# Kernel tuning notes

Measured on AMD Instinct MI355X. Metric: run time of the kernel, lower is better.

Reference implementation:

```python
import jax, jax.numpy as jnp
import numpy as np

N = 10000
E = 320000
D = 256
EPS = 1e-5

def layer_norm(x, g, b):
    mu = jnp.mean(x, axis=-1, keepdims=True)
    var = jnp.mean(jnp.square(x - mu), axis=-1, keepdims=True)
    return (x - mu) * jax.lax.rsqrt(var + EPS) * g + b

def linear(x, w, b):
    # w: [in, out]
    return x @ w + b

def setup_inputs() -> dict:
    key = jax.random.key(0)
    ks = jax.random.split(key, 20)
    s = 1.0 / np.sqrt(D)
    inp = {
        'x': jax.random.normal(ks[0], (N, D), jnp.float32),
        'edge_index': jax.random.randint(ks[1], (2, E), 0, N, jnp.int64),
        'edge_weight': jax.random.normal(ks[2], (E,), jnp.float32),
        'wq': jax.random.normal(ks[3], (D, D), jnp.float32) * s,
        'bq': jnp.zeros((D,), jnp.float32),
        'wk': jax.random.normal(ks[4], (D, D), jnp.float32) * s,
        'bk': jnp.zeros((D,), jnp.float32),
        'wv': jax.random.normal(ks[5], (D, D), jnp.float32) * s,
        'bv': jnp.zeros((D,), jnp.float32),
        'ws': jax.random.normal(ks[6], (D, D), jnp.float32) * s,
        'bs': jnp.zeros((D,), jnp.float32),
        'we': jax.random.normal(ks[7], (1, 1), jnp.float32),
        'be': jnp.zeros((1,), jnp.float32),
        'g1': jnp.ones((D,), jnp.float32),
        'b1': jnp.zeros((D,), jnp.float32),
        'g2': jnp.ones((D,), jnp.float32),
        'b2': jnp.zeros((D,), jnp.float32),
        'w_ff1': jax.random.normal(ks[8], (D, 2 * D), jnp.float32) * s,
        'b_ff1': jnp.zeros((2 * D,), jnp.float32),
        'w_ff2': jax.random.normal(ks[9], (2 * D, D), jnp.float32) * (1.0 / np.sqrt(2 * D)),
        'b_ff2': jnp.zeros((D,), jnp.float32),
    }
    return inp

def reference(x, edge_index, edge_weight, wq, bq, wk, bk, wv, bv, ws, bs, we, be,
              g1, b1, g2, b2, w_ff1, b_ff1, w_ff2, b_ff2):
    n = x.shape[0]
    scale = x.shape[-1] ** (-0.5)
    q = linear(x, wq, bq)
    k = linear(x, wk, bk)
    v = linear(x, wv, bv)
    src, dst = edge_index[0], edge_index[1]
    # per-edge attention scores: dot(q[dst], k[src]) * scale
    scores = jnp.sum(q[dst] * k[src], axis=-1) * scale
    scores = scores + (edge_weight[:, None] @ we + be)[:, 0]
    # two-pass segment softmax over dst
    seg_max = jax.ops.segment_max(scores, dst, num_segments=n)
    exp_s = jnp.exp(scores - seg_max[dst])
    denom = jax.ops.segment_sum(exp_s, dst, num_segments=n)
    attn = exp_s / jnp.maximum(denom[dst], 1e-12)
    # scatter-add weighted messages
    message = v[src] * attn[:, None]  # [E, D]
    out = jax.ops.segment_sum(message, dst, num_segments=n)
    x = layer_norm(x + out + linear(x, ws, bs), g1, b1)
    ffn = linear(jax.nn.gelu(linear(x, w_ff1, b_ff1)), w_ff2, b_ff2)
    x = layer_norm(x + ffn, g2, b2)
    return x
```

## Files before the change

kernel.cpp:

```cpp
#include <hip/hip_runtime.h>
#include <math.h>

#define N_NODES 10000
#define N_EDGES 320000
#define DIM 256
#define BCAP 128

#define P_PARTS 250
#define NPP 40
#define PCAP 2048
#define EPT 16

typedef __attribute__((ext_vector_type(8))) short bf16x8;
typedef __attribute__((ext_vector_type(4))) float fx4;

typedef __attribute__((address_space(3))) unsigned lds_u32;
typedef __attribute__((address_space(1))) const unsigned gbl_u32;


__device__ __forceinline__ float gelu_tanh(float x) {
  const float k0 = 0.7978845608028654f;
  float x3 = x * x * x;
  return 0.5f * x * (1.0f + tanhf(k0 * (x + 0.044715f * x3)));
}

__device__ __forceinline__ unsigned short f2bf(float f) {
  unsigned u = __float_as_uint(f);
  unsigned r = 0x7FFFu + ((u >> 16) & 1u);
  return (unsigned short)((u + r) >> 16);
}

__device__ __forceinline__ float bf_lo(unsigned u) { return __uint_as_float(u << 16); }
__device__ __forceinline__ float bf_hi(unsigned u) { return __uint_as_float(u & 0xFFFF0000u); }


#define SEG_QKVS 262144
#define SEG_FF1 131072
#define SEG_FF2 131072
#define SEG_BIAS 1024
#define SEG_CONV 320000
#define SEG_ZCNT 256
#define PREP_TOTAL (SEG_QKVS + SEG_FF1 + SEG_FF2 + SEG_BIAS + SEG_CONV + SEG_ZCNT)

__global__ __launch_bounds__(256) void prep_all_kernel(
    const float* __restrict__ wq, const float* __restrict__ wk,
    const float* __restrict__ wv, const float* __restrict__ ws,
    const float* __restrict__ bq, const float* __restrict__ bk,
    const float* __restrict__ bv, const float* __restrict__ bs,
    const float* __restrict__ wff1, const float* __restrict__ wff2,
    const float* __restrict__ x,
    unsigned short* __restrict__ wt_qkvs, float* __restrict__ bias_qkvs,
    unsigned short* __restrict__ wt_ff1, unsigned short* __restrict__ wt_ff2,
    unsigned short* __restrict__ xb, unsigned* __restrict__ pcnt) {
  int id = blockIdx.x * 256 + threadIdx.x;
  if (id < SEG_QKVS) {
    const int n = id >> 8, k = id & 255;
    const float* w = (n < 256) ? wq : (n < 512) ? wk : (n < 768) ? wv : ws;
    wt_qkvs[id] = f2bf(w[k * 256 + (n & 255)]);
    return;
  }
  id -= SEG_QKVS;
  if (id < SEG_FF1) {
    const int n = id >> 8, k = id & 255;
    wt_ff1[id] = f2bf(wff1[k * 512 + n]);
    return;
  }
  id -= SEG_FF1;
  if (id < SEG_FF2) {
    const int n = id >> 9, k = id & 511;
    wt_ff2[id] = f2bf(wff2[k * 256 + n]);
    return;
  }
  id -= SEG_FF2;
  if (id < SEG_BIAS) {
    bias_qkvs[id] = (id < 256) ? bq[id] : (id < 512) ? bk[id & 255]
                    : (id < 768) ? bv[id & 255] : bs[id & 255];
    return;
  }
  id -= SEG_BIAS;
  if (id < SEG_CONV) {
    const int base = id * 8;
    float4 a = *(const float4*)(x + base);
    float4 b = *(const float4*)(x + base + 4);
    unsigned short h[8] = {f2bf(a.x), f2bf(a.y), f2bf(a.z), f2bf(a.w),
                           f2bf(b.x), f2bf(b.y), f2bf(b.z), f2bf(b.w)};
    *(uint4*)(xb + base) = *(const uint4*)h;
    return;
  }
  id -= SEG_CONV;
  if (id < SEG_ZCNT) pcnt[id] = 0u;
}

__global__ __launch_bounds__(512) void scatter_p1(
    const int* __restrict__ ei, const float* __restrict__ ew,
    const float* __restrict__ we, const float* __restrict__ be,
    unsigned* __restrict__ pcnt, uint2* __restrict__ pbuf) {
  __shared__ unsigned lcnt[P_PARTS];
  __shared__ unsigned lbase[P_PARTS];
  const int tid = threadIdx.x;
  for (int i = tid; i < P_PARTS; i += 512) lcnt[i] = 0;
  __syncthreads();
  const float wes = we[0], bes = be[0];
  const int e0 = blockIdx.x * (512 * EPT);

  unsigned pp[EPT];
  unsigned rr[EPT];
  unsigned sv[EPT];
  float ebv[EPT];
#pragma unroll
  for (int j = 0; j < EPT; j++) {
    const int e = e0 + j * 512 + tid;
    pp[j] = 0;
    rr[j] = 0xFFFFFFFFu;
    if (e < N_EDGES) {
      const int dst = ei[N_EDGES + e];
      const int src = ei[e];
      const int p = dst / NPP;
      sv[j] = (unsigned)dst | ((unsigned)src << 16);
      ebv[j] = fmaf(ew[e], wes, bes);
      pp[j] = (unsigned)p;
      rr[j] = atomicAdd(&lcnt[p], 1u);
    }
  }
  __syncthreads();
  for (int i = tid; i < P_PARTS; i += 512) {
    const unsigned c = lcnt[i];
    lbase[i] = c ? atomicAdd(&pcnt[i], c) : 0u;
  }
  __syncthreads();
#pragma unroll
  for (int j = 0; j < EPT; j++) {
    if (rr[j] != 0xFFFFFFFFu) {
      const unsigned pos = lbase[pp[j]] + rr[j];
      if (pos < PCAP) {
        uint2 rec;
        rec.x = sv[j];
        rec.y = __float_as_uint(ebv[j]);
        pbuf[(size_t)pp[j] * PCAP + pos] = rec;
      }
    }
  }
}

__global__ __launch_bounds__(256) void scatter_p2(
    const unsigned* __restrict__ pcnt, const uint2* __restrict__ pbuf,
    unsigned* __restrict__ cnt, uint2* __restrict__ es_csr) {
  __shared__ unsigned lcnt[NPP];
  const int p = blockIdx.x;
  const int tid = threadIdx.x;
  if (tid < NPP) lcnt[tid] = 0;
  __syncthreads();
  const int n0 = p * NPP;
  const int tot = min((int)pcnt[p], PCAP);
  for (int i = tid; i < tot; i += 256) {
    const uint2 rec = pbuf[(size_t)p * PCAP + i];
    const int dst = (int)(rec.x & 0xFFFFu);
    const int src = (int)(rec.x >> 16);
    const unsigned r = atomicAdd(&lcnt[dst - n0], 1u);
    if (r < BCAP) {
      uint2 o;
      o.x = (unsigned)src;
      o.y = rec.y;
      es_csr[(size_t)dst * BCAP + r] = o;
    }
  }
  __syncthreads();
  if (tid < NPP) cnt[n0 + tid] = lcnt[tid];
}

template <int GELU, int WF32, int WB16, int SPLIT>
__global__ __launch_bounds__(256) void mfma_gemm(
    const unsigned short* __restrict__ A, int lda,
    const unsigned short* __restrict__ Bt,
    const float* __restrict__ bias,
    const float* __restrict__ xres,
    float* __restrict__ C, int ldc,
    unsigned short* __restrict__ Cb, int ldcb,
    int M, int K) {
  __shared__ char lds[65536];
  const int tid = threadIdx.x;

  const int l = tid & 63;
  const int wid = tid >> 6;
  const int wrow = (wid & 1) * 64;
  const int wcol = (wid >> 1) * 64;
  const int bm = blockIdx.y * 128;
  const int bn = blockIdx.x * 128;

  fx4 acc[4][4];
#pragma unroll
  for (int i = 0; i < 4; i++)
#pragma unroll
    for (int j = 0; j < 4; j++) acc[i][j] = (fx4)(0.0f);

#define STAGE(BUFOFF, KB)                                                      \
  {                                                                            \
    _Pragma("unroll") for (int i = 0; i < 4; i++) {                            \
      const int id = i * 256 + tid;                                            \
      const int row = id >> 3;                                                 \
      const int ccs = (id & 7) ^ (row & 7);                                    \
      __builtin_amdgcn_global_load_lds(                                        \
          (gbl_u32*)(A + (size_t)(bm + row) * lda + (KB) + ccs * 8),           \
          (lds_u32*)(lds + (BUFOFF) + id * 16), 16, 0, 0);                     \
    }                                                                          \
    _Pragma("unroll") for (int i = 0; i < 4; i++) {                            \
      const int id = i * 256 + tid;                                            \
      const int row = id >> 3;                                                 \
      const int ccs = (id & 7) ^ (row & 7);                                    \
      __builtin_amdgcn_global_load_lds(                                        \
          (gbl_u32*)(Bt + (size_t)(bn + row) * K + (KB) + ccs * 8),            \
          (lds_u32*)(lds + (BUFOFF) + 16384 + id * 16), 16, 0, 0);             \
    }                                                                          \
  }

  STAGE(0, 0);

  unsigned cur = 0;
  for (int kb = 0; kb < K; kb += 64) {
    if (kb + 64 < K) {
      STAGE((cur ^ 1) * 32768, kb + 64);
      asm volatile("s_waitcnt vmcnt(8)" ::: "memory");
    } else {
      asm volatile("s_waitcnt vmcnt(0)" ::: "memory");
    }
    __builtin_amdgcn_s_barrier();
    __builtin_amdgcn_sched_barrier(0);

    const char* As = lds + cur * 32768;
    const char* Bs = As + 16384;
#pragma unroll
    for (int kk = 0; kk < 2; kk++) {
      const int kbyte = (kk * 64 + ((l >> 4) << 4)) ^ ((l & 7) << 4);
      bf16x8 af[4], bg[4];
#pragma unroll
      for (int f = 0; f < 4; f++) {
        const int ar = wrow + f * 16 + (l & 15);
        af[f] = *(const bf16x8*)(As + ar * 128 + kbyte);
        const int br = wcol + f * 16 + (l & 15);
        bg[f] = *(const bf16x8*)(Bs + br * 128 + kbyte);
      }
#pragma unroll
      for (int fr = 0; fr < 4; fr++)
#pragma unroll
        for (int fc = 0; fc < 4; fc++)
          acc[fr][fc] = __builtin_amdgcn_mfma_f32_16x16x32_bf16(
              bg[fc], af[fr], acc[fr][fc], 0, 0, 0);
    }
    __builtin_amdgcn_s_barrier();
    cur ^= 1;
  }
#undef STAGE

  const int seg = bn >> 8;
#pragma unroll
  for (int fr = 0; fr < 4; fr++) {
    const int m = bm + wrow + fr * 16 + (l & 15);
    if (m < M) {
#pragma unroll
      for (int fc = 0; fc < 4; fc++) {
        const int n0 = bn + wcol + fc * 16 + ((l >> 4) << 2);
        const float4 b4 = *(const float4*)(bias + n0);
        fx4 v = acc[fr][fc];
        float o0 = v[0] + b4.x;
        float o1 = v[1] + b4.y;
        float o2 = v[2] + b4.z;
        float o3 = v[3] + b4.w;
        if (GELU) {
          o0 = gelu_tanh(o0); o1 = gelu_tanh(o1);
          o2 = gelu_tanh(o2); o3 = gelu_tanh(o3);
        }
        if (SPLIT) {
          const int nn = n0 & 255;
          if (seg == 3) {
            const float4 xr = *(const float4*)(xres + (size_t)m * 256 + nn);
            float4 w;
            w.x = o0 + xr.x; w.y = o1 + xr.y; w.z = o2 + xr.z; w.w = o3 + xr.w;
            *(float4*)(C + (size_t)m * 256 + nn) = w;
          } else {
            uint2 pk;
            pk.x = (unsigned)f2bf(o0) | ((unsigned)f2bf(o1) << 16);
            pk.y = (unsigned)f2bf(o2) | ((unsigned)f2bf(o3) << 16);
            *(uint2*)(Cb + (size_t)seg * (N_NODES * DIM) + (size_t)m * 256 + nn) = pk;
          }
        } else {
          if (WF32) {
            float4 w; w.x = o0; w.y = o1; w.z = o2; w.w = o3;
            *(float4*)(C + (size_t)m * ldc + n0) = w;
          }
          if (WB16) {
            uint2 pk;
            pk.x = (unsigned)f2bf(o0) | ((unsigned)f2bf(o1) << 16);
            pk.y = (unsigned)f2bf(o2) | ((unsigned)f2bf(o3) << 16);
            *(uint2*)(Cb + (size_t)m * ldcb + n0) = pk;
          }
        }
      }
    }
  }
}

__global__ __launch_bounds__(64) void agg_fused_kernel(
    const unsigned* __restrict__ cnt, const uint2* __restrict__ es_csr,
    const unsigned short* __restrict__ qb,
    const unsigned short* __restrict__ kb, const unsigned short* __restrict__ vb,
    const float* __restrict__ sbuf,
    const float* __restrict__ g, const float* __restrict__ b,
    float* __restrict__ out, unsigned short* __restrict__ outb) {
  const int node = blockIdx.x;
  const int lane = threadIdx.x;
  const int grp = lane >> 4;
  const int t = lane & 15;
  const int start = node * BCAP;
  const int deg = min((int)cnt[node], BCAP);
  const int end = start + deg;

  const uint4 qA = *(const uint4*)(qb + (size_t)node * 256 + t * 16);
  const uint4 qB = *(const uint4*)(qb + (size_t)node * 256 + t * 16 + 8);
  float qf[16];
  qf[0] = bf_lo(qA.x);  qf[1] = bf_hi(qA.x);
  qf[2] = bf_lo(qA.y);  qf[3] = bf_hi(qA.y);
  qf[4] = bf_lo(qA.z);  qf[5] = bf_hi(qA.z);
  qf[6] = bf_lo(qA.w);  qf[7] = bf_hi(qA.w);
  qf[8] = bf_lo(qB.x);  qf[9] = bf_hi(qB.x);
  qf[10] = bf_lo(qB.y); qf[11] = bf_hi(qB.y);
  qf[12] = bf_lo(qB.z); qf[13] = bf_hi(qB.z);
  qf[14] = bf_lo(qB.w); qf[15] = bf_hi(qB.w);

  float m = -3.4e38f, dsum = 0.f;
  float a0 = 0.f, a1 = 0.f, a2 = 0.f, a3 = 0.f;

  int ea = start + grp * 2;
  int eb_ = ea + 1;
  bool va = ea < end, vbd = eb_ < end;
  int sa = 0, sb = 0;
  float ba = 0.f, bb = 0.f;
  if (va) { const uint2 es = es_csr[ea]; sa = (int)es.x; ba = __uint_as_float(es.y); }
  if (vbd) { const uint2 es = es_csr[eb_]; sb = (int)es.x; bb = __uint_as_float(es.y); }
  uint4 kAa = *(const uint4*)(kb + (size_t)sa * 256 + t * 16);
  uint4 kBa = *(const uint4*)(kb + (size_t)sa * 256 + t * 16 + 8);
  uint4 kAb = *(const uint4*)(kb + (size_t)sb * 256 + t * 16);
  uint4 kBb = *(const uint4*)(kb + (size_t)sb * 256 + t * 16 + 8);

  for (int base = start; base < end; base += 8) {
    const int s0 = __shfl(sa, 0), s1 = __shfl(sa, 16);
    const int s2 = __shfl(sa, 32), s3 = __shfl(sa, 48);
    const int s4 = __shfl(sb, 0), s5 = __shfl(sb, 16);
    const int s6 = __shfl(sb, 32), s7 = __shfl(sb, 48);
    const uint2 v0 = *(const uint2*)(vb + (size_t)s0 * 256 + lane * 4);
    const uint2 v1 = *(const uint2*)(vb + (size_t)s1 * 256 + lane * 4);
    const uint2 v2 = *(const uint2*)(vb + (size_t)s2 * 256 + lane * 4);
    const uint2 v3 = *(const uint2*)(vb + (size_t)s3 * 256 + lane * 4);
    const uint2 v4 = *(const uint2*)(vb + (size_t)s4 * 256 + lane * 4);
    const uint2 v5 = *(const uint2*)(vb + (size_t)s5 * 256 + lane * 4);
    const uint2 v6 = *(const uint2*)(vb + (size_t)s6 * 256 + lane * 4);
    const uint2 v7 = *(const uint2*)(vb + (size_t)s7 * 256 + lane * 4);

    const int na = base + 8 + grp * 2;
    const int nb = na + 1;
    const bool va_n = na < end, vb_n = nb < end;
    int sa_n = 0, sb_n = 0;
    float ba_n = 0.f, bb_n = 0.f;
    if (va_n) { const uint2 es = es_csr[na]; sa_n = (int)es.x; ba_n = __uint_as_float(es.y); }
    if (vb_n) { const uint2 es = es_csr[nb]; sb_n = (int)es.x; bb_n = __uint_as_float(es.y); }

    float da = qf[0] * bf_lo(kAa.x);
    float db = qf[0] * bf_lo(kAb.x);
    da = fmaf(qf[1], bf_hi(kAa.x), da);  db = fmaf(qf[1], bf_hi(kAb.x), db);
    da = fmaf(qf[2], bf_lo(kAa.y), da);  db = fmaf(qf[2], bf_lo(kAb.y), db);
    da = fmaf(qf[3], bf_hi(kAa.y), da);  db = fmaf(qf[3], bf_hi(kAb.y), db);
    da = fmaf(qf[4], bf_lo(kAa.z), da);  db = fmaf(qf[4], bf_lo(kAb.z), db);
    da = fmaf(qf[5], bf_hi(kAa.z), da);  db = fmaf(qf[5], bf_hi(kAb.z), db);
    da = fmaf(qf[6], bf_lo(kAa.w), da);  db = fmaf(qf[6], bf_lo(kAb.w), db);
    da = fmaf(qf[7], bf_hi(kAa.w), da);  db = fmaf(qf[7], bf_hi(kAb.w), db);
    da = fmaf(qf[8], bf_lo(kBa.x), da);  db = fmaf(qf[8], bf_lo(kBb.x), db);
    da = fmaf(qf[9], bf_hi(kBa.x), da);  db = fmaf(qf[9], bf_hi(kBb.x), db);
    da = fmaf(qf[10], bf_lo(kBa.y), da); db = fmaf(qf[10], bf_lo(kBb.y), db);
    da = fmaf(qf[11], bf_hi(kBa.y), da); db = fmaf(qf[11], bf_hi(kBb.y), db);
    da = fmaf(qf[12], bf_lo(kBa.z), da); db = fmaf(qf[12], bf_lo(kBb.z), db);
    da = fmaf(qf[13], bf_hi(kBa.z), da); db = fmaf(qf[13], bf_hi(kBb.z), db);
    da = fmaf(qf[14], bf_lo(kBa.w), da); db = fmaf(qf[14], bf_lo(kBb.w), db);
    da = fmaf(qf[15], bf_hi(kBa.w), da); db = fmaf(qf[15], bf_hi(kBb.w), db);
    da += __shfl_xor(da, 1);  db += __shfl_xor(db, 1);
    da += __shfl_xor(da, 2);  db += __shfl_xor(db, 2);
    da += __shfl_xor(da, 4);  db += __shfl_xor(db, 4);
    da += __shfl_xor(da, 8);  db += __shfl_xor(db, 8);
    const float sca = va ? fmaf(da, 0.0625f, ba) : -3.4e38f;
    const float scb = vbd ? fmaf(db, 0.0625f, bb) : -3.4e38f;

    const uint4 kAa_n = *(const uint4*)(kb + (size_t)sa_n * 256 + t * 16);
    const uint4 kBa_n = *(const uint4*)(kb + (size_t)sa_n * 256 + t * 16 + 8);
    const uint4 kAb_n = *(const uint4*)(kb + (size_t)sb_n * 256 + t * 16);
    const uint4 kBb_n = *(const uint4*)(kb + (size_t)sb_n * 256 + t * 16 + 8);

    const float c0 = __shfl(sca, 0), c1 = __shfl(sca, 16);
    const float c2 = __shfl(sca, 32), c3 = __shfl(sca, 48);
    const float c4 = __shfl(scb, 0), c5 = __shfl(scb, 16);
    const float c6 = __shfl(scb, 32), c7 = __shfl(scb, 48);

    const float mx = fmaxf(fmaxf(fmaxf(c0, c1), fmaxf(c2, c3)),
                           fmaxf(fmaxf(c4, c5), fmaxf(c6, c7)));
    const float mn = fmaxf(m, mx);
    const float scale = __expf(m - mn);
    const float w0 = __expf(c0 - mn), w1 = __expf(c1 - mn);
    const float w2 = __expf(c2 - mn), w3 = __expf(c3 - mn);
    const float w4 = __expf(c4 - mn), w5 = __expf(c5 - mn);
    const float w6 = __expf(c6 - mn), w7 = __expf(c7 - mn);
    dsum = fmaf(dsum, scale, ((w0 + w1) + (w2 + w3)) + ((w4 + w5) + (w6 + w7)));

    float t0 = a0 * scale;
    t0 = fmaf(w0, bf_lo(v0.x), t0); t0 = fmaf(w1, bf_lo(v1.x), t0);
    t0 = fmaf(w2, bf_lo(v2.x), t0); t0 = fmaf(w3, bf_lo(v3.x), t0);
    t0 = fmaf(w4, bf_lo(v4.x), t0); t0 = fmaf(w5, bf_lo(v5.x), t0);
    t0 = fmaf(w6, bf_lo(v6.x), t0); t0 = fmaf(w7, bf_lo(v7.x), t0);
    a0 = t0;
    float t1 = a1 * scale;
    t1 = fmaf(w0, bf_hi(v0.x), t1); t1 = fmaf(w1, bf_hi(v1.x), t1);
    t1 = fmaf(w2, bf_hi(v2.x), t1); t1 = fmaf(w3, bf_hi(v3.x), t1);
    t1 = fmaf(w4, bf_hi(v4.x), t1); t1 = fmaf(w5, bf_hi(v5.x), t1);
    t1 = fmaf(w6, bf_hi(v6.x), t1); t1 = fmaf(w7, bf_hi(v7.x), t1);
    a1 = t1;
    float t2 = a2 * scale;
    t2 = fmaf(w0, bf_lo(v0.y), t2); t2 = fmaf(w1, bf_lo(v1.y), t2);
    t2 = fmaf(w2, bf_lo(v2.y), t2); t2 = fmaf(w3, bf_lo(v3.y), t2);
    t2 = fmaf(w4, bf_lo(v4.y), t2); t2 = fmaf(w5, bf_lo(v5.y), t2);
    t2 = fmaf(w6, bf_lo(v6.y), t2); t2 = fmaf(w7, bf_lo(v7.y), t2);
    a2 = t2;
    float t3 = a3 * scale;
    t3 = fmaf(w0, bf_hi(v0.y), t3); t3 = fmaf(w1, bf_hi(v1.y), t3);
    t3 = fmaf(w2, bf_hi(v2.y), t3); t3 = fmaf(w3, bf_hi(v3.y), t3);
    t3 = fmaf(w4, bf_hi(v4.y), t3); t3 = fmaf(w5, bf_hi(v5.y), t3);
    t3 = fmaf(w6, bf_hi(v6.y), t3); t3 = fmaf(w7, bf_hi(v7.y), t3);
    a3 = t3;
    m = mn;

    sa = sa_n; sb = sb_n;
    ba = ba_n; bb = bb_n;
    va = va_n; vbd = vb_n;
    kAa = kAa_n; kBa = kBa_n;
    kAb = kAb_n; kBb = kBb_n;
  }
  const float inv = 1.0f / fmaxf(dsum, 1e-12f);

  const float4 sv = *(const float4*)(sbuf + (size_t)node * 256 + lane * 4);
  float r0 = a0 * inv + sv.x;
  float r1 = a1 * inv + sv.y;
  float r2 = a2 * inv + sv.z;
  float r3 = a3 * inv + sv.w;

  float sum = r0 + r1 + r2 + r3;
#pragma unroll
  for (int off = 32; off > 0; off >>= 1) sum += __shfl_xor(sum, off);
  const float mu = sum * (1.0f / 256.0f);
  const float d0 = r0 - mu, d1 = r1 - mu, d2 = r2 - mu, d3 = r3 - mu;
  float vs = d0 * d0 + d1 * d1 + d2 * d2 + d3 * d3;
#pragma unroll
  for (int off = 32; off > 0; off >>= 1) vs += __shfl_xor(vs, off);
  const float rs = rsqrtf(vs * (1.0f / 256.0f) + 1e-5f);

  const float4 gv = *(const float4*)(g + lane * 4);
  const float4 bv = *(const float4*)(b + lane * 4);
  float4 o;
  o.x = d0 * rs * gv.x + bv.x;
  o.y = d1 * rs * gv.y + bv.y;
  o.z = d2 * rs * gv.z + bv.z;
  o.w = d3 * rs * gv.w + bv.w;
  *(float4*)(out + (size_t)node * 256 + lane * 4) = o;
  uint2 pk;
  pk.x = (unsigned)f2bf(o.x) | ((unsigned)f2bf(o.y) << 16);
  pk.y = (unsigned)f2bf(o.z) | ((unsigned)f2bf(o.w) << 16);
  *(uint2*)(outb + (size_t)node * 256 + lane * 4) = pk;
}


__global__ __launch_bounds__(256) void ln2_kernel(
    const float* __restrict__ x1, const float* __restrict__ y,
    const float* __restrict__ g, const float* __restrict__ b,
    float* __restrict__ out) {
  __shared__ float red[4];
  const int row = blockIdx.x;
  const int t = threadIdx.x;
  float v = x1[(size_t)row * 256 + t] + y[(size_t)row * 256 + t];
  float s = v;
#pragma unroll
  for (int off = 32; off > 0; off >>= 1) s += __shfl_xor(s, off);
  if ((t & 63) == 0) red[t >> 6] = s;
  __syncthreads();
  float tot = red[0] + red[1] + red[2] + red[3];
  __syncthreads();
  const float mu = tot * (1.0f / 256.0f);
  const float d = v - mu;
  float vs = d * d;
#pragma unroll
  for (int off = 32; off > 0; off >>= 1) vs += __shfl_xor(vs, off);
  if ((t & 63) == 0) red[t >> 6] = vs;
  __syncthreads();
  float vtot = red[0] + red[1] + red[2] + red[3];
  const float r = rsqrtf(vtot * (1.0f / 256.0f) + 1e-5f);
  out[(size_t)row * 256 + t] = d * r * g[t] + b[t];
}


extern "C" void kernel_launch(void* const* d_in, const int* in_sizes, int n_in,
                              void* d_out, int out_size, void* d_ws,
                              size_t ws_size, hipStream_t stream) {
  const float* x = (const float*)d_in[0];
  const int* ei = (const int*)d_in[1];
  const float* ew = (const float*)d_in[2];
  const float* wq = (const float*)d_in[3];
  const float* bq = (const float*)d_in[4];
  const float* wk = (const float*)d_in[5];
  const float* bk = (const float*)d_in[6];
  const float* wv = (const float*)d_in[7];
  const float* bv = (const float*)d_in[8];
  const float* wsm = (const float*)d_in[9];
  const float* bs = (const float*)d_in[10];
  const float* we = (const float*)d_in[11];
  const float* be = (const float*)d_in[12];
  const float* g1 = (const float*)d_in[13];
  const float* b1 = (const float*)d_in[14];
  const float* g2 = (const float*)d_in[15];
  const float* b2 = (const float*)d_in[16];
  const float* wff1 = (const float*)d_in[17];
  const float* bff1 = (const float*)d_in[18];
  const float* wff2 = (const float*)d_in[19];
  const float* bff2 = (const float*)d_in[20];
  float* out = (float*)d_out;

  unsigned short* qb = (unsigned short*)d_ws;
  unsigned short* kbp = qb + 2560000;
  unsigned short* vbp = qb + 5120000;
  float* sbuf = (float*)(qb + 7680000);
  uint2* es_csr = (uint2*)(sbuf + 2560000);
  unsigned* cnt = (unsigned*)(es_csr + (size_t)N_NODES * BCAP);
  float* x1 = (float*)(cnt + N_NODES);
  float* y = x1 + 2560000;
  unsigned short* x1b = (unsigned short*)(y + 2560000);
  unsigned short* h_b = x1b + 2560000;
  unsigned short* xb = h_b;
  unsigned short* wt_qkvs = h_b + 5120000;
  unsigned short* wt_ff1 = wt_qkvs + 262144;
  unsigned short* wt_ff2 = wt_ff1 + 131072;
  float* bias_qkvs = (float*)(wt_ff2 + 131072);
  unsigned* pcnt = (unsigned*)(bias_qkvs + 1024);
  uint2* pbuf = (uint2*)(pcnt + 256);

  dim3 blk(256);
  const int mb = (N_NODES + 127) / 128;

  prep_all_kernel<<<(PREP_TOTAL + 255) / 256, blk, 0, stream>>>(
      wq, wk, wv, wsm, bq, bk, bv, bs, wff1, wff2, x,
      wt_qkvs, bias_qkvs, wt_ff1, wt_ff2, xb, pcnt);

  scatter_p1<<<(N_EDGES + 512 * EPT - 1) / (512 * EPT), dim3(512), 0, stream>>>(
      ei, ew, we, be, pcnt, pbuf);
  scatter_p2<<<P_PARTS, blk, 0, stream>>>(pcnt, pbuf, cnt, es_csr);

  mfma_gemm<0, 0, 0, 1><<<dim3(8, mb), blk, 0, stream>>>(
      xb, 256, wt_qkvs, bias_qkvs, x, sbuf, 0, qb, 0, N_NODES, 256);

  agg_fused_kernel<<<N_NODES, dim3(64), 0, stream>>>(
      cnt, es_csr, qb, kbp, vbp, sbuf, g1, b1, x1, x1b);

  mfma_gemm<1, 0, 1, 0><<<dim3(4, mb), blk, 0, stream>>>(
      x1b, 256, wt_ff1, bff1, nullptr, (float*)nullptr, 0, h_b, 512, N_NODES, 256);

  mfma_gemm<0, 1, 0, 0><<<dim3(2, mb), blk, 0, stream>>>(
      h_b, 512, wt_ff2, bff2, nullptr, y, 256, (unsigned short*)nullptr, 0, N_NODES, 512);

  ln2_kernel<<<N_NODES, blk, 0, stream>>>(x1, y, g2, b2, out);
}
```

Measured before the change: 133.6 us.

## Use 64x64 split-K MFMA GEMM for FFN2 with reduction fused into LN2

Replaces the 128-row-tile FFN2 GEMM (only 2x79 blocks) with a 64x64-tile kernel that splits K=512 into two halves across blockIdx.z, giving 4x157x2 blocks for better CU occupancy. Each half writes a separate fp32 partial, with bias applied only in the first, and ln2 sums both partials. This adds a 10MB partial write and an extra read in LN2. The last row tile reads past N_NODES in A (10000 is not a multiple of 64), though stores are guarded.

```diff
diff --git a/kernel.cpp b/kernel.cpp
--- a/kernel.cpp
+++ b/kernel.cpp
@@ -299,6 +299,108 @@
   }
 }
 
+__global__ __launch_bounds__(256) void mfma_gemm64_splitk(
+    const unsigned short* __restrict__ A, int lda,
+    const unsigned short* __restrict__ Bt, int ldb,
+    const float* __restrict__ bias,
+    float* __restrict__ C,
+    int M, int kLen) {
+  __shared__ char lds[32768];
+  const int tid = threadIdx.x;
+  const int l = tid & 63;
+  const int wid = tid >> 6;
+  const int wrow = (wid & 1) * 32;
+  const int wcol = (wid >> 1) * 32;
+  const int bm = blockIdx.y * 64;
+  const int bn = blockIdx.x * 64;
+  const int kOff = blockIdx.z * kLen;
+  const float bmul = (blockIdx.z == 0) ? 1.0f : 0.0f;
+  float* Cz = C + (size_t)blockIdx.z * (N_NODES * DIM);
+
+  fx4 acc[2][2];
+#pragma unroll
+  for (int i = 0; i < 2; i++)
+#pragma unroll
+    for (int j = 0; j < 2; j++) acc[i][j] = (fx4)(0.0f);
+
+#define STAGE64(BUFOFF, KB)                                                    \
+  {                                                                            \
+    _Pragma("unroll") for (int i = 0; i < 2; i++) {                            \
+      const int id = i * 256 + tid;                                            \
+      const int row = id >> 3;                                                 \
+      const int ccs = (id & 7) ^ (row & 7);                                    \
+      __builtin_amdgcn_global_load_lds(                                        \
+          (gbl_u32*)(A + (size_t)(bm + row) * lda + kOff + (KB) + ccs * 8),    \
+          (lds_u32*)(lds + (BUFOFF) + id * 16), 16, 0, 0);                     \
+    }                                                                          \
+    _Pragma("unroll") for (int i = 0; i < 2; i++) {                            \
+      const int id = i * 256 + tid;                                            \
+      const int row = id >> 3;                                                 \
+      const int ccs = (id & 7) ^ (row & 7);                                    \
+      __builtin_amdgcn_global_load_lds(                                        \
+          (gbl_u32*)(Bt + (size_t)(bn + row) * ldb + kOff + (KB) + ccs * 8),   \
+          (lds_u32*)(lds + (BUFOFF) + 8192 + id * 16), 16, 0, 0);              \
+    }                                                                          \
+  }
+
+  STAGE64(0, 0);
+
+  unsigned cur = 0;
+  for (int kb = 0; kb < kLen; kb += 64) {
+    if (kb + 64 < kLen) {
+      STAGE64((cur ^ 1) * 16384, kb + 64);
+      asm volatile("s_waitcnt vmcnt(4)" ::: "memory");
+    } else {
+      asm volatile("s_waitcnt vmcnt(0)" ::: "memory");
+    }
+    __builtin_amdgcn_s_barrier();
+    __builtin_amdgcn_sched_barrier(0);
+
+    const char* As = lds + cur * 16384;
+    const char* Bs = As + 8192;
+#pragma unroll
+    for (int kk = 0; kk < 2; kk++) {
+      const int kbyte = (kk * 64 + ((l >> 4) << 4)) ^ ((l & 7) << 4);
+      bf16x8 af[2], bg[2];
+#pragma unroll
+      for (int f = 0; f < 2; f++) {
+        const int ar = wrow + f * 16 + (l & 15);
+        af[f] = *(const bf16x8*)(As + ar * 128 + kbyte);
+        const int br = wcol + f * 16 + (l & 15);
+        bg[f] = *(const bf16x8*)(Bs + br * 128 + kbyte);
+      }
+#pragma unroll
+      for (int fr = 0; fr < 2; fr++)
+#pragma unroll
+        for (int fc = 0; fc < 2; fc++)
+          acc[fr][fc] = __builtin_amdgcn_mfma_f32_16x16x32_bf16(
+              bg[fc], af[fr], acc[fr][fc], 0, 0, 0);
+    }
+    __builtin_amdgcn_s_barrier();
+    cur ^= 1;
+  }
+#undef STAGE64
+
+#pragma unroll
+  for (int fr = 0; fr < 2; fr++) {
+    const int m = bm + wrow + fr * 16 + (l & 15);
+    if (m < M) {
+#pragma unroll
+      for (int fc = 0; fc < 2; fc++) {
+        const int n0 = bn + wcol + fc * 16 + ((l >> 4) << 2);
+        const float4 b4 = *(const float4*)(bias + n0);
+        fx4 v = acc[fr][fc];
+        float4 w;
+        w.x = fmaf(b4.x, bmul, v[0]);
+        w.y = fmaf(b4.y, bmul, v[1]);
+        w.z = fmaf(b4.z, bmul, v[2]);
+        w.w = fmaf(b4.w, bmul, v[3]);
+        *(float4*)(Cz + (size_t)m * DIM + n0) = w;
+      }
+    }
+  }
+}
+
 __global__ __launch_bounds__(64) void agg_fused_kernel(
     const unsigned* __restrict__ cnt, const uint2* __restrict__ es_csr,
     const unsigned short* __restrict__ qb,
@@ -474,12 +576,14 @@
 
 __global__ __launch_bounds__(256) void ln2_kernel(
     const float* __restrict__ x1, const float* __restrict__ y,
+    const float* __restrict__ y2,
     const float* __restrict__ g, const float* __restrict__ b,
     float* __restrict__ out) {
   __shared__ float red[4];
   const int row = blockIdx.x;
   const int t = threadIdx.x;
-  float v = x1[(size_t)row * 256 + t] + y[(size_t)row * 256 + t];
+  const size_t idx = (size_t)row * 256 + t;
+  float v = x1[idx] + y[idx] + y2[idx];
   float s = v;
 #pragma unroll
   for (int off = 32; off > 0; off >>= 1) s += __shfl_xor(s, off);
@@ -496,7 +600,7 @@
   __syncthreads();
   float vtot = red[0] + red[1] + red[2] + red[3];
   const float r = rsqrtf(vtot * (1.0f / 256.0f) + 1e-5f);
-  out[(size_t)row * 256 + t] = d * r * g[t] + b[t];
+  out[idx] = d * r * g[t] + b[t];
 }
 
 
@@ -543,9 +647,14 @@
   float* bias_qkvs = (float*)(wt_ff2 + 131072);
   unsigned* pcnt = (unsigned*)(bias_qkvs + 1024);
   uint2* pbuf = (uint2*)(pcnt + 256);
+  float* ysp = (float*)(pbuf + (size_t)P_PARTS * PCAP);
+
+  float* yk = ysp;
+  float* y2 = ysp + 2560000;
 
   dim3 blk(256);
-  const int mb = (N_NODES + 127) / 128;
+  const int mb128 = (N_NODES + 127) / 128;
+  const int mb64 = (N_NODES + 63) / 64;
 
   prep_all_kernel<<<(PREP_TOTAL + 255) / 256, blk, 0, stream>>>(
       wq, wk, wv, wsm, bq, bk, bv, bs, wff1, wff2, x,
@@ -555,17 +664,17 @@
       ei, ew, we, be, pcnt, pbuf);
   scatter_p2<<<P_PARTS, blk, 0, stream>>>(pcnt, pbuf, cnt, es_csr);
 
-  mfma_gemm<0, 0, 0, 1><<<dim3(8, mb), blk, 0, stream>>>(
+  mfma_gemm<0, 0, 0, 1><<<dim3(8, mb128), blk, 0, stream>>>(
       xb, 256, wt_qkvs, bias_qkvs, x, sbuf, 0, qb, 0, N_NODES, 256);
 
   agg_fused_kernel<<<N_NODES, dim3(64), 0, stream>>>(
       cnt, es_csr, qb, kbp, vbp, sbuf, g1, b1, x1, x1b);
 
-  mfma_gemm<1, 0, 1, 0><<<dim3(4, mb), blk, 0, stream>>>(
+  mfma_gemm<1, 0, 1, 0><<<dim3(4, mb128), blk, 0, stream>>>(
       x1b, 256, wt_ff1, bff1, nullptr, (float*)nullptr, 0, h_b, 512, N_NODES, 256);
 
-  mfma_gemm<0, 1, 0, 0><<<dim3(2, mb), blk, 0, stream>>>(
-      h_b, 512, wt_ff2, bff2, nullptr, y, 256, (unsigned short*)nullptr, 0, N_NODES, 512);
-
-  ln2_kernel<<<N_NODES, blk, 0, stream>>>(x1, y, g2, b2, out);
-}
+  mfma_gemm64_splitk<<<dim3(4, mb64, 2), blk, 0, stream>>>(
+      h_b, 512, wt_ff2, 512, bff2, yk, N_NODES, 256);
+
+  ln2_kernel<<<N_NODES, blk, 0, stream>>>(x1, yk, y2, g2, b2, out);
+}
```

New measurement: 138.9 us. 3.9% more time.
